# Kernel optimization log

Measured on AMD Instinct MI355X. Metric: run time of the kernel, lower is better.

The kernel has to match this reference:

```python
import jax, jax.numpy as jnp
import numpy as np

B, H, W, C, NUM_HEADS = 32, 8, 128, 512, 8
HK, WK = 7, 11  # local_k
N = H * W
HEAD_DIM = C // NUM_HEADS
SCALE = HEAD_DIM ** (-0.5)


def make_local_mask():
    # key (i,j) is visible to query (h,w) iff i+HK//2 in [h, h+HK) and j+WK//2 in [w, w+WK)
    dh = jnp.arange(H)[None, :] - jnp.arange(H)[:, None] + HK // 2  # [H(query), H(key)]
    dw = jnp.arange(W)[None, :] - jnp.arange(W)[:, None] + WK // 2  # [W(query), W(key)]
    ok_h = (dh >= 0) & (dh < HK)
    ok_w = (dw >= 0) & (dw < WK)
    ok = ok_h[:, None, :, None] & ok_w[None, :, None, :]  # [H,W,H,W]
    return jnp.where(ok.reshape(N, N), 0.0, -jnp.inf).astype(jnp.float32)


def setup_inputs() -> dict:
    key = jax.random.key(0)
    k1, k2, k3 = jax.random.split(key, 3)
    s = C ** (-0.5)
    return {
        "x": jax.random.normal(k1, (B, N, C), dtype=jnp.float32),
        "w_qkv": jax.random.normal(k2, (C, 3 * C), dtype=jnp.float32) * s,
        "w_proj": jax.random.normal(k3, (C, C), dtype=jnp.float32) * s,
        "b_proj": jnp.zeros((C,), dtype=jnp.float32),
    }


def reference(x, w_qkv, w_proj, b_proj):
    mask = make_local_mask()  # [N, N], 0 in window, -inf outside
    b, n, c = x.shape
    qkv = (x @ w_qkv).reshape(b, n, 3, NUM_HEADS, HEAD_DIM)
    qkv = jnp.transpose(qkv, (2, 0, 3, 1, 4))  # [3, B, heads, N, head_dim]
    q, k, v = qkv[0], qkv[1], qkv[2]
    attn = jnp.einsum('bhqd,bhkd->bhqk', q, k) * SCALE + mask
    attn = jax.nn.softmax(attn, axis=-1)
    out = jnp.einsum('bhqk,bhkd->bhqd', attn, v)
    out = jnp.transpose(out, (0, 2, 1, 3)).reshape(b, n, c)
    return out @ w_proj + b_proj
```

## Files before the change

### kernel.cpp

```cpp
#include <hip/hip_runtime.h>

#define Bsz   32
#define Hh    8
#define Ww    128
#define Cc    512
#define NHEAD 8
#define HD    64
#define NN    1024
#define SCALE 0.125f
#define ROWS  1536
#define ROWSP 1568

typedef _Float16 f16x8 __attribute__((ext_vector_type(8)));
typedef float    f32x4 __attribute__((ext_vector_type(4)));

__device__ __forceinline__ void gload16(const _Float16* g, _Float16* l) {
#if __has_builtin(__builtin_amdgcn_global_load_lds)
  __builtin_amdgcn_global_load_lds(
      (const __attribute__((address_space(1))) unsigned int*)g,
      (__attribute__((address_space(3))) unsigned int*)l, 16, 0, 0);
#else
  *(uint4*)l = *(const uint4*)g;
#endif
}

__global__ __launch_bounds__(256) void cvt_f32_f16(
    const float* __restrict__ in, _Float16* __restrict__ out, int n8) {
  const int i = blockIdx.x * 256 + threadIdx.x;
  if (i < n8) {
    const float4 f0 = ((const float4*)in)[(size_t)i * 2];
    const float4 f1 = ((const float4*)in)[(size_t)i * 2 + 1];
    union { _Float16 h[8]; uint4 u; } pk;
    pk.h[0] = (_Float16)f0.x; pk.h[1] = (_Float16)f0.y;
    pk.h[2] = (_Float16)f0.z; pk.h[3] = (_Float16)f0.w;
    pk.h[4] = (_Float16)f1.x; pk.h[5] = (_Float16)f1.y;
    pk.h[6] = (_Float16)f1.z; pk.h[7] = (_Float16)f1.w;
    ((uint4*)out)[i] = pk.u;
  }
}

__global__ __launch_bounds__(256) void tcvt(
    const float* __restrict__ in, _Float16* __restrict__ out, int Nn, int K) {
  const int id = blockIdx.x * 256 + threadIdx.x;
  if (id < Nn * K) {
    const int n = id / K, k = id - n * K;
    out[id] = (_Float16)in[(size_t)k * Nn + n];
  }
}

template<bool OUT_F16, bool HAS_BIAS>
__global__ __launch_bounds__(512, 2) void gemm_mfma(
    const _Float16* __restrict__ A,
    const _Float16* __restrict__ BT,
    const float* __restrict__ bias,
    void* __restrict__ Cout,
    int nbx, int Nn, int K, int ldc)
{
  __shared__ _Float16 As[2][256 * 32];
  __shared__ _Float16 Bs[2][256 * 32];

  const int wg    = blockIdx.x;
  const int chunk = gridDim.x >> 3;
  const int nid   = (wg & 7) * chunk + (wg >> 3);
  const int bn    = (nid % nbx) * 256;
  const int bm    = (nid / nbx) * 256;

  const int t  = threadIdx.x;
  const int l  = t & 63, wv = t >> 6;
  const int wr = wv >> 2, wc = wv & 3;

  f32x4 acc[8][4] = {};

  auto stage = [&](int k0, int pb) {
#pragma unroll
    for (int q = 0; q < 2; ++q) {
      const int c   = t + q * 512;
      const int row = c >> 2, k4 = c & 3;
      const int ks  = (k4 ^ ((row >> 1) & 3)) << 3;
      gload16(A  + (size_t)(bm + row) * K + k0 + ks, &As[pb][c * 8]);
      gload16(BT + (size_t)(bn + row) * K + k0 + ks, &Bs[pb][c * 8]);
    }
  };

  const int nt = K / 32;

  stage(0, 0);
  __syncthreads();

  const int rA   = l & 15;
  const int kofs = ((l >> 4) * 8) ^ (((rA >> 1) & 3) << 3);

  int buf = 0;
  for (int tt = 0; tt < nt; ++tt) {
    if (tt + 1 < nt) stage((tt + 1) * 32, buf ^ 1);

    f16x8 bF[4];
#pragma unroll
    for (int jj = 0; jj < 4; ++jj)
      bF[jj] = *(const f16x8*)&Bs[buf][(wc * 64 + jj * 16 + rA) * 32 + kofs];
#pragma unroll
    for (int i = 0; i < 8; ++i) {
      const f16x8 aF = *(const f16x8*)&As[buf][(wr * 128 + i * 16 + rA) * 32 + kofs];
#pragma unroll
      for (int jj = 0; jj < 4; ++jj)
        acc[i][jj] = __builtin_amdgcn_mfma_f32_16x16x32_f16(aF, bF[jj], acc[i][jj], 0, 0, 0);
    }

    __syncthreads();
    buf ^= 1;
  }

  const int lc = l & 15, lr4 = (l >> 4) * 4;
#pragma unroll
  for (int i = 0; i < 8; ++i) {
    const size_t row0 = (size_t)(bm + wr * 128 + i * 16 + lr4);
#pragma unroll
    for (int jj = 0; jj < 4; ++jj) {
      const int col = bn + wc * 64 + jj * 16 + lc;
      const float bv = HAS_BIAS ? bias[col] : 0.f;
#pragma unroll
      for (int r = 0; r < 4; ++r) {
        const float v = acc[i][jj][r] + bv;
        if (OUT_F16)
          ((_Float16*)Cout)[(row0 + r) * ldc + col] = (_Float16)v;
        else
          ((float*)Cout)[(row0 + r) * ldc + col] = v;
      }
    }
  }
}

__global__ __launch_bounds__(512, 4) void local_attn_mfma(
    const _Float16* __restrict__ qkv, _Float16* __restrict__ outh)
{
  const int wg  = blockIdx.x;
  const int nid = ((wg & 7) << 7) + (wg >> 3);
  const int hp = nid & 3, head = (nid >> 2) & 7, b = nid >> 5;
  const int h0 = hp * 2;

  const int t = threadIdx.x;
  const int wv = t >> 6, l = t & 63;
  const int g = l >> 4, c = l & 15;
  const int w0 = wv * 16;
  const int kb = min(max(w0 - 8, 0), 96);

  __shared__ _Float16 Ksh[8192];
  __shared__ _Float16 Vsh[64 * 132];
  __shared__ _Float16 Pbuf[8][576];

  const _Float16* qb = qkv + (size_t)b * NN * ROWSP;

  f16x8 qF[2][2];
#pragma unroll
  for (int hi = 0; hi < 2; ++hi) {
    const _Float16* Qg = qb + (size_t)((h0 + hi) * Ww + w0 + c) * ROWSP + head * HD;
    qF[hi][0] = *(const f16x8*)&Qg[g * 8];
    qF[hi][1] = *(const f16x8*)&Qg[32 + g * 8];
  }

  float mbias[2][4];
#pragma unroll
  for (int tt = 0; tt < 2; ++tt)
#pragma unroll
    for (int r = 0; r < 4; ++r) {
      const int kcol = kb + 16 * tt + 4 * g + r;
      const int qq   = w0 + c;
      mbias[tt][r] = (kcol >= qq - 5 && kcol <= qq + 5) ? 0.f : -1e30f;
    }

  const int r0 = max(0, h0 - 3), r1 = min(Hh - 1, h0 + 4);
  float s_part[2] = {0.f, 0.f};
  f32x4 accO[2][4] = {};

  const int dd = t & 7, cg = (t & 255) >> 3;

  for (int kr = r0; kr <= r1; ++kr) {
    __syncthreads();
    if (t < 256) {
      const _Float16* Kg = qb + (size_t)(kr * Ww) * ROWSP + Cc + head * HD;
#pragma unroll
      for (int i = 0; i < 4; ++i) {
        const int o   = (i * 4 + wv) * 64 + l;
        const int col = o >> 3, dc = o & 7;
        gload16(Kg + (size_t)col * ROWSP + ((dc ^ (col & 7)) << 3), &Ksh[o * 8]);
      }
    } else {
      f16x8 vr[4];
      const _Float16* Vg = qb + (size_t)(kr * Ww + cg * 4) * ROWSP + 2 * Cc + head * HD + dd * 8;
#pragma unroll
      for (int i = 0; i < 4; ++i)
        vr[i] = *(const f16x8*)&Vg[(size_t)i * ROWSP];
#pragma unroll
      for (int e = 0; e < 8; ++e) {
        union { _Float16 hh[4]; uint2 u; } pk;
        pk.hh[0] = vr[0][e]; pk.hh[1] = vr[1][e];
        pk.hh[2] = vr[2][e]; pk.hh[3] = vr[3][e];
        *(uint2*)&Vsh[(dd * 8 + e) * 132 + cg * 4] = pk.u;
      }
    }
    __syncthreads();

#pragma unroll
    for (int hi = 0; hi < 2; ++hi) {
      const int hq = h0 + hi;
      if (kr < hq - 3 || kr > hq + 3) continue;

      f32x4 accS[2] = {};
      __builtin_amdgcn_s_setprio(1);
#pragma unroll
      for (int tt = 0; tt < 2; ++tt) {
        const int col = kb + 16 * tt + c;
#pragma unroll
        for (int s = 0; s < 2; ++s) {
          const f16x8 kF = *(const f16x8*)&Ksh[col * 64 + (((s * 4 + g) ^ (c & 7)) << 3)];
          accS[tt] = __builtin_amdgcn_mfma_f32_16x16x32_f16(kF, qF[hi][s], accS[tt], 0, 0, 0);
        }
      }
      __builtin_amdgcn_s_setprio(0);

#pragma unroll
      for (int tt = 0; tt < 2; ++tt) {
        float p0 = __expf(fminf(__builtin_fmaf(accS[tt][0], SCALE, mbias[tt][0]), 11.f));
        float p1 = __expf(fminf(__builtin_fmaf(accS[tt][1], SCALE, mbias[tt][1]), 11.f));
        float p2 = __expf(fminf(__builtin_fmaf(accS[tt][2], SCALE, mbias[tt][2]), 11.f));
        float p3 = __expf(fminf(__builtin_fmaf(accS[tt][3], SCALE, mbias[tt][3]), 11.f));
        s_part[hi] += (p0 + p1) + (p2 + p3);
        union { _Float16 hh[4]; uint2 u; } pk;
        pk.hh[0] = (_Float16)p0; pk.hh[1] = (_Float16)p1;
        pk.hh[2] = (_Float16)p2; pk.hh[3] = (_Float16)p3;
        *(uint2*)&Pbuf[wv][c * 36 + 16 * tt + 4 * g] = pk.u;
      }

      union { f16x8 v; uint2 u2[2]; } pF;
      {
        const _Float16* pp = &Pbuf[wv][c * 36 + g * 8];
        pF.u2[0] = *(const uint2*)pp;
        pF.u2[1] = *(const uint2*)(pp + 4);
      }
      __builtin_amdgcn_s_setprio(1);
#pragma unroll
      for (int jj = 0; jj < 4; ++jj) {
        union { f16x8 v; uint2 u2[2]; } vF;
        const _Float16* vp = &Vsh[(16 * jj + c) * 132 + kb + g * 8];
        vF.u2[0] = *(const uint2*)vp;
        vF.u2[1] = *(const uint2*)(vp + 4);
        accO[hi][jj] = __builtin_amdgcn_mfma_f32_16x16x32_f16(pF.v, vF.v, accO[hi][jj], 0, 0, 0);
      }
      __builtin_amdgcn_s_setprio(0);
    }
  }

#pragma unroll
  for (int hi = 0; hi < 2; ++hi) {
    float s_run = s_part[hi];
    s_run += __shfl_xor(s_run, 16);
    s_run += __shfl_xor(s_run, 32);
    _Float16* ob = outh + ((size_t)b * NN + (h0 + hi) * Ww + w0) * Cc + head * HD;
#pragma unroll
    for (int r = 0; r < 4; ++r) {
      const float sr  = __shfl(s_run, 4 * g + r, 16);
      const float inv = 1.f / sr;
      const int q = 4 * g + r;
#pragma unroll
      for (int jj = 0; jj < 4; ++jj)
        ob[(size_t)q * Cc + 16 * jj + c] = (_Float16)(accO[hi][jj][r] * inv);
    }
  }
}

extern "C" void kernel_launch(void* const* d_in, const int* in_sizes, int n_in,
                              void* d_out, int out_size, void* d_ws, size_t ws_size,
                              hipStream_t stream)
{
  const float* x      = (const float*)d_in[0];
  const float* w_qkv  = (const float*)d_in[1];
  const float* w_proj = (const float*)d_in[2];
  const float* b_proj = (const float*)d_in[3];
  float* out = (float*)d_out;

  const int M = Bsz * NN;
  char* ws = (char*)d_ws;
  _Float16* xh    = (_Float16*)ws;
  _Float16* qkvh  = (_Float16*)(ws + 33554432);
  _Float16* attnh = (_Float16*)(ws + 136314880);
  _Float16* wqT   = (_Float16*)(ws + 169869312);
  _Float16* wpT   = (_Float16*)(ws + 171442176);

  cvt_f32_f16<<<(M * Cc / 8 + 255) / 256, 256, 0, stream>>>(x, xh, M * Cc / 8);
  tcvt<<<(ROWS * Cc + 255) / 256, 256, 0, stream>>>(w_qkv, wqT, ROWS, Cc);
  tcvt<<<(Cc * Cc + 255) / 256, 256, 0, stream>>>(w_proj, wpT, Cc, Cc);

  gemm_mfma<true, false><<<(ROWS / 256) * (M / 256), 512, 0, stream>>>(
      xh, wqT, nullptr, qkvh, ROWS / 256, ROWS, Cc, ROWSP);

  local_attn_mfma<<<(Hh / 2) * NHEAD * Bsz, 512, 0, stream>>>(qkvh, attnh);

  gemm_mfma<false, true><<<(Cc / 256) * (M / 256), 512, 0, stream>>>(
      attnh, wpT, b_proj, out, Cc / 256, Cc, Cc, Cc);
}
```

Baseline: 183.5 us.

## Restructure GEMM into eight-phase pipelined schedule with 64-wide K tiles

The GEMM kernel now uses K tiles of 64 instead of 32, split into quarter-tile stages whose global-to-LDS loads are issued several phases ahead. Each iteration interleaves LDS fragment loads, MFMA blocks and barriers across eight phases, with explicit vmcnt/lgkmcnt waits and raised scheduling priority around the MFMA blocks. Each wave's output quadrant is also remapped, and the LDS swizzle changes to an 8-way XOR. The aim is to hide global-load latency and cut barrier stalls in the two projection GEMMs, at the cost of doubled LDS use and fragile hand-placed wait counts.

```diff
diff --git a/kernel.cpp b/kernel.cpp
--- a/kernel.cpp
+++ b/kernel.cpp
@@ -49,15 +49,15 @@
 }
 
 template<bool OUT_F16, bool HAS_BIAS>
-__global__ __launch_bounds__(512, 2) void gemm_mfma(
+__global__ __launch_bounds__(512, 2) void gemm8p(
     const _Float16* __restrict__ A,
     const _Float16* __restrict__ BT,
     const float* __restrict__ bias,
     void* __restrict__ Cout,
     int nbx, int Nn, int K, int ldc)
 {
-  __shared__ _Float16 As[2][256 * 32];
-  __shared__ _Float16 Bs[2][256 * 32];
+  __shared__ _Float16 As[2][256 * 64];
+  __shared__ _Float16 Bs[2][256 * 64];
 
   const int wg    = blockIdx.x;
   const int chunk = gridDim.x >> 3;
@@ -71,63 +71,125 @@
 
   f32x4 acc[8][4] = {};
 
-  auto stage = [&](int k0, int pb) {
-#pragma unroll
-    for (int q = 0; q < 2; ++q) {
-      const int c   = t + q * 512;
-      const int row = c >> 2, k4 = c & 3;
-      const int ks  = (k4 ^ ((row >> 1) & 3)) << 3;
-      gload16(A  + (size_t)(bm + row) * K + k0 + ks, &As[pb][c * 8]);
-      gload16(BT + (size_t)(bn + row) * K + k0 + ks, &Bs[pb][c * 8]);
-    }
+  const int srow0 = t >> 3;
+  const int soff0 = (((t & 7) ^ (srow0 & 7)) << 3);
+  const int srow1 = (t + 512) >> 3;
+  const int soff1 = (((t & 7) ^ (srow1 & 7)) << 3);
+  const int smax  = (K >> 4) - 1;
+
+  auto stage = [&](int s) {
+    if (s > smax) return;
+    const int kt = s >> 2, h = s & 3;
+    const int k0 = kt * 64, buf = kt & 1;
+    _Float16* dst = ((h & 1) ? Bs[buf] : As[buf]) + (h >> 1) * 8192;
+    const _Float16* src = (h & 1) ? (BT + (size_t)(bn + (h >> 1) * 128) * K)
+                                  : (A  + (size_t)(bm + (h >> 1) * 128) * K);
+    gload16(src + (size_t)srow0 * K + k0 + soff0, dst + t * 8);
+    gload16(src + (size_t)srow1 * K + k0 + soff1, dst + t * 8 + 4096);
   };
 
-  const int nt = K / 32;
-
-  stage(0, 0);
-  __syncthreads();
-
-  const int rA   = l & 15;
-  const int kofs = ((l >> 4) * 8) ^ (((rA >> 1) & 3) << 3);
-
-  int buf = 0;
-  for (int tt = 0; tt < nt; ++tt) {
-    if (tt + 1 < nt) stage((tt + 1) * 32, buf ^ 1);
-
-    f16x8 bF[4];
-#pragma unroll
-    for (int jj = 0; jj < 4; ++jj)
-      bF[jj] = *(const f16x8*)&Bs[buf][(wc * 64 + jj * 16 + rA) * 32 + kofs];
-#pragma unroll
-    for (int i = 0; i < 8; ++i) {
-      const f16x8 aF = *(const f16x8*)&As[buf][(wr * 128 + i * 16 + rA) * 32 + kofs];
-#pragma unroll
-      for (int jj = 0; jj < 4; ++jj)
-        acc[i][jj] = __builtin_amdgcn_mfma_f32_16x16x32_f16(aF, bF[jj], acc[i][jj], 0, 0, 0);
-    }
-
-    __syncthreads();
-    buf ^= 1;
-  }
+  const int rA = l & 15, rx = rA & 7, kgb = l >> 4;
+
+  auto loadA = [&](int buf, int rh, f16x8* aF) {
+#pragma unroll
+    for (int i = 0; i < 4; ++i) {
+      const int row = rh * 128 + wr * 64 + i * 16 + rA;
+#pragma unroll
+      for (int kh = 0; kh < 2; ++kh)
+        aF[i * 2 + kh] = *(const f16x8*)&As[buf][row * 64 + (((kgb + 4 * kh) ^ rx) << 3)];
+    }
+  };
+  auto loadB = [&](int buf, int ch, f16x8* bF) {
+#pragma unroll
+    for (int j = 0; j < 2; ++j) {
+      const int col = ch * 128 + wc * 32 + j * 16 + rA;
+#pragma unroll
+      for (int kh = 0; kh < 2; ++kh)
+        bF[j * 2 + kh] = *(const f16x8*)&Bs[buf][col * 64 + (((kgb + 4 * kh) ^ rx) << 3)];
+    }
+  };
+  auto mma16 = [&](const f16x8* aF, const f16x8* bF, int rh, int ch) {
+    __builtin_amdgcn_s_setprio(1);
+#pragma unroll
+    for (int i = 0; i < 4; ++i)
+#pragma unroll
+      for (int j = 0; j < 2; ++j)
+#pragma unroll
+        for (int kh = 0; kh < 2; ++kh)
+          acc[rh * 4 + i][ch * 2 + j] = __builtin_amdgcn_mfma_f32_16x16x32_f16(
+              aF[i * 2 + kh], bF[j * 2 + kh], acc[rh * 4 + i][ch * 2 + j], 0, 0, 0);
+    __builtin_amdgcn_s_setprio(0);
+  };
+
+#define PH_SYNC()                                          \
+  __builtin_amdgcn_s_barrier();                            \
+  asm volatile("s_waitcnt lgkmcnt(0)" ::: "memory");       \
+  __builtin_amdgcn_sched_barrier(0)
+
+  stage(0); stage(1); stage(2); stage(3); stage(4); stage(5);
+  asm volatile("s_waitcnt vmcnt(4)" ::: "memory");
+  __builtin_amdgcn_s_barrier();
+
+  const int nIter = K / 128;
+  f16x8 aF[8], bF0[4], bF1[4];
+
+  for (int it = 0; it < nIter; ++it) {
+    const int sb = 6 + it * 8;
+    const bool lastIt = (it == nIter - 1);
+
+    loadA(0, 0, aF); loadB(0, 0, bF0); stage(sb + 0);
+    PH_SYNC(); mma16(aF, bF0, 0, 0); __builtin_amdgcn_s_barrier();
+
+    loadB(0, 1, bF1); stage(sb + 1);
+    PH_SYNC(); mma16(aF, bF1, 0, 1); __builtin_amdgcn_s_barrier();
+
+    loadA(0, 1, aF); stage(sb + 2);
+    PH_SYNC(); mma16(aF, bF0, 1, 0); __builtin_amdgcn_s_barrier();
+
+    stage(sb + 3);
+    PH_SYNC(); mma16(aF, bF1, 1, 1);
+    if (lastIt) asm volatile("s_waitcnt vmcnt(0)" ::: "memory");
+    else        asm volatile("s_waitcnt vmcnt(4)" ::: "memory");
+    __builtin_amdgcn_s_barrier();
+
+    loadA(1, 0, aF); loadB(1, 0, bF0); stage(sb + 4);
+    PH_SYNC(); mma16(aF, bF0, 0, 0); __builtin_amdgcn_s_barrier();
+
+    loadB(1, 1, bF1); stage(sb + 5);
+    PH_SYNC(); mma16(aF, bF1, 0, 1); __builtin_amdgcn_s_barrier();
+
+    loadA(1, 1, aF); stage(sb + 6);
+    PH_SYNC(); mma16(aF, bF0, 1, 0); __builtin_amdgcn_s_barrier();
+
+    stage(sb + 7);
+    PH_SYNC(); mma16(aF, bF1, 1, 1);
+    if (!lastIt) asm volatile("s_waitcnt vmcnt(4)" ::: "memory");
+    __builtin_amdgcn_s_barrier();
+  }
+#undef PH_SYNC
 
   const int lc = l & 15, lr4 = (l >> 4) * 4;
 #pragma unroll
-  for (int i = 0; i < 8; ++i) {
-    const size_t row0 = (size_t)(bm + wr * 128 + i * 16 + lr4);
-#pragma unroll
-    for (int jj = 0; jj < 4; ++jj) {
-      const int col = bn + wc * 64 + jj * 16 + lc;
-      const float bv = HAS_BIAS ? bias[col] : 0.f;
-#pragma unroll
-      for (int r = 0; r < 4; ++r) {
-        const float v = acc[i][jj][r] + bv;
-        if (OUT_F16)
-          ((_Float16*)Cout)[(row0 + r) * ldc + col] = (_Float16)v;
-        else
-          ((float*)Cout)[(row0 + r) * ldc + col] = v;
-      }
-    }
-  }
+  for (int rh = 0; rh < 2; ++rh)
+#pragma unroll
+    for (int i = 0; i < 4; ++i) {
+      const size_t row0 = (size_t)(bm + rh * 128 + wr * 64 + i * 16 + lr4);
+#pragma unroll
+      for (int ch = 0; ch < 2; ++ch)
+#pragma unroll
+        for (int j = 0; j < 2; ++j) {
+          const int col = bn + ch * 128 + wc * 32 + j * 16 + lc;
+          const float bv = HAS_BIAS ? bias[col] : 0.f;
+#pragma unroll
+          for (int r = 0; r < 4; ++r) {
+            const float v = acc[rh * 4 + i][ch * 2 + j][r] + bv;
+            if (OUT_F16)
+              ((_Float16*)Cout)[(row0 + r) * ldc + col] = (_Float16)v;
+            else
+              ((float*)Cout)[(row0 + r) * ldc + col] = v;
+          }
+        }
+    }
 }
 
 __global__ __launch_bounds__(512, 4) void local_attn_mfma(
@@ -290,11 +352,11 @@
   tcvt<<<(ROWS * Cc + 255) / 256, 256, 0, stream>>>(w_qkv, wqT, ROWS, Cc);
   tcvt<<<(Cc * Cc + 255) / 256, 256, 0, stream>>>(w_proj, wpT, Cc, Cc);
 
-  gemm_mfma<true, false><<<(ROWS / 256) * (M / 256), 512, 0, stream>>>(
+  gemm8p<true, false><<<(ROWS / 256) * (M / 256), 512, 0, stream>>>(
       xh, wqT, nullptr, qkvh, ROWS / 256, ROWS, Cc, ROWSP);
 
   local_attn_mfma<<<(Hh / 2) * NHEAD * Bsz, 512, 0, stream>>>(qkvh, attnh);
 
-  gemm_mfma<false, true><<<(Cc / 256) * (M / 256), 512, 0, stream>>>(
+  gemm8p<false, true><<<(Cc / 256) * (M / 256), 512, 0, stream>>>(
       attnh, wpT, b_proj, out, Cc / 256, Cc, Cc, Cc);
 }
```

Result: faster. 166.5 us (-9.3%).
